# Optimization experiments

Measured on AMD Instinct MI355X. Metric: run time of the kernel, lower is better.

The kernel has to match this reference:

```python
import jax, jax.numpy as jnp
import numpy as np

NUM_HEADS = 8
OUT_FEATURES = 64
ALPHA = 0.2


def setup_inputs() -> dict:
    key = jax.random.key(0)
    k1, k2, k3, k4 = jax.random.split(key, 4)
    B, N, E, F_IN = 2, 8192, 4096, 256
    x = jax.random.normal(k1, (B, N, F_IN), dtype=jnp.float32)
    H = jax.random.uniform(k2, (N, E), dtype=jnp.float32)
    # xavier-like scaled params
    W = jax.random.normal(k3, (F_IN, OUT_FEATURES * NUM_HEADS), dtype=jnp.float32) * 0.05
    a_vertices = jax.random.normal(k4, (OUT_FEATURES, 1), dtype=jnp.float32) * 0.1
    return {"x": x, "H": H, "W": W, "a_vertices": a_vertices}


def reference(x, H, W, a_vertices):
    B, N, _ = x.shape
    # Wh: (B, N, heads, out)
    Wh = jnp.matmul(x, W).reshape(B, N, NUM_HEADS, OUT_FEATURES)
    # per-node, per-head attention logit: (B, N, heads)
    av = jax.nn.leaky_relu(jnp.einsum('bnhd,d->bnh', Wh, a_vertices[:, 0]), ALPHA)
    # edge attention: softmax over edges (torch dim=0 of (E, heads))
    ae = jax.nn.softmax(jnp.einsum('ne,bnh->beh', H, av), axis=1)  # (B, E, heads)
    # aggregate node features onto edges: (B, E, heads, out)
    m = jnp.einsum('ne,bnhd->behd', H, Wh)
    # scatter back to nodes with edge-attention weighting: (B, N, heads, out)
    out = jnp.einsum('ne,beh,behd->bnhd', H, ae, m)
    return out.reshape(B, N, NUM_HEADS * OUT_FEATURES)
```

## Files before the change

kernel.cpp:

```cpp
#include <hip/hip_runtime.h>

#define N_NODES 8192
#define N_EDGES 4096
#define F_INS   256
#define HEADS   8
#define DOUT    64
#define HDIM    512
#define CCOMB   1024
#define BATCH   2

typedef __bf16 bf16x8 __attribute__((ext_vector_type(8)));
typedef __bf16 bf16x4 __attribute__((ext_vector_type(4)));
typedef float  f32x4  __attribute__((ext_vector_type(4)));

__device__ __forceinline__ void gld_lds16(const __bf16* g, __bf16* l) {
    __builtin_amdgcn_global_load_lds(
        (const __attribute__((address_space(1))) void*)g,
        (__attribute__((address_space(3))) void*)l, 16, 0, 0);
}

__launch_bounds__(256, 4)
__global__ void convert_H_logits_kernel(const float* __restrict__ H,
                                        const float* __restrict__ av,
                                        __bf16* __restrict__ Hb,
                                        __bf16* __restrict__ HbT,
                                        float* __restrict__ plog) {
    __shared__ __align__(16) char smem[33280];
    float* lav = (float*)smem;
    __bf16 (*tile)[32][132] = (__bf16(*)[32][132])(smem + 16384);
    float* red = (float*)smem;

    int t = threadIdx.x;
    int e0 = blockIdx.x * 128;
    int n0 = blockIdx.y * 256;
    int equad = t & 31, r0 = t >> 5;
    int lane = t & 63, wv = t >> 6;

    for (int p = t; p < 4096; p += 256) {
        int n = p >> 4, q = p & 15, b = q >> 3, h = q & 7;
        lav[p] = av[(size_t)b * (N_NODES * 8) + (size_t)(n0 + n) * 8 + h];
    }

    const float* hbase = H + (size_t)n0 * N_EDGES + e0 + equad * 4;
    __bf16* hb_base = Hb + (size_t)n0 * N_EDGES + e0 + equad * 4;

    f32x4 acc[4][4] = {};

    __syncthreads();

    float4 v[4];
    for (int g = 0; g < 8; ++g) {
        int nb = g * 32;
#pragma unroll
        for (int k = 0; k < 4; ++k) {
            int n = nb + r0 + 8 * k;
            v[k] = *(const float4*)(hbase + (size_t)n * N_EDGES);
        }
        if (g > 0) {
            int pb = (g - 1) & 1, pnb = (g - 1) * 32;
#pragma unroll
            for (int s = 0; s < 2; ++s) {
                int id = s * 256 + t;
                int er = id >> 2, oct = id & 3;
                bf16x8 val;
#pragma unroll
                for (int j = 0; j < 8; ++j) val[j] = tile[pb][oct * 8 + j][er];
                *(bf16x8*)(HbT + (size_t)(e0 + er) * N_NODES + n0 + pnb + oct * 8) = val;
            }
        }
        int buf = g & 1;
#pragma unroll
        for (int k = 0; k < 4; ++k) {
            int n = nb + r0 + 8 * k;
            const f32x4* lrow = (const f32x4*)&lav[n * 16];
            float4 vv = v[k];
#pragma unroll
            for (int qq = 0; qq < 4; ++qq) {
                f32x4 l = lrow[qq];
                acc[0][qq] += l * vv.x;
                acc[1][qq] += l * vv.y;
                acc[2][qq] += l * vv.z;
                acc[3][qq] += l * vv.w;
            }
            bf16x4 hb;
            hb.x = (__bf16)vv.x; hb.y = (__bf16)vv.y;
            hb.z = (__bf16)vv.z; hb.w = (__bf16)vv.w;
            *(bf16x4*)(hb_base + (size_t)n * N_EDGES) = hb;
            *(bf16x4*)&tile[buf][r0 + 8 * k][equad * 4] = hb;
        }
        __syncthreads();
    }
    {
        int pnb = 7 * 32;
#pragma unroll
        for (int s = 0; s < 2; ++s) {
            int id = s * 256 + t;
            int er = id >> 2, oct = id & 3;
            bf16x8 val;
#pragma unroll
            for (int j = 0; j < 8; ++j) val[j] = tile[1][oct * 8 + j][er];
            *(bf16x8*)(HbT + (size_t)(e0 + er) * N_NODES + n0 + pnb + oct * 8) = val;
        }
    }

#pragma unroll
    for (int ec = 0; ec < 4; ++ec)
#pragma unroll
        for (int qq = 0; qq < 4; ++qq)
#pragma unroll
            for (int qi = 0; qi < 4; ++qi)
                acc[ec][qq][qi] += __shfl_xor(acc[ec][qq][qi], 32, 64);

    __syncthreads();
    if (lane < 32) {
#pragma unroll
        for (int qq = 0; qq < 4; ++qq)
#pragma unroll
            for (int qi = 0; qi < 4; ++qi) {
                f32x4 tmp = {acc[0][qq][qi], acc[1][qq][qi],
                             acc[2][qq][qi], acc[3][qq][qi]};
                *(f32x4*)&red[wv * 2048 + (qq * 4 + qi) * 128 + equad * 4] = tmp;
            }
    }
    __syncthreads();
#pragma unroll
    for (int s = 0; s < 8; ++s) {
        int id = s * 256 + t;
        int q = id >> 7, el = id & 127;
        float sum = red[q * 128 + el] + red[2048 + q * 128 + el] +
                    red[4096 + q * 128 + el] + red[6144 + q * 128 + el];
        plog[((size_t)blockIdx.y * 16 + q) * N_EDGES + e0 + el] = sum;
    }
}

__launch_bounds__(256)
__global__ void reduce_logits_kernel(const float* __restrict__ plog,
                                     float* __restrict__ logits) {
    int id = blockIdx.x * 256 + threadIdx.x;
    int q = id >> 12, e = id & 4095;
    float s = 0.f;
#pragma unroll
    for (int nb = 0; nb < 32; ++nb)
        s += plog[((size_t)nb * 16 + q) * N_EDGES + e];
    logits[(size_t)q * N_EDGES + e] = s;
}

__launch_bounds__(256)
__global__ void wbt_kernel(const float* __restrict__ W, __bf16* __restrict__ WbT) {
    int i = blockIdx.x * 256 + threadIdx.x;
    int c = i >> 8, f = i & 255;
    WbT[i] = (__bf16)W[(size_t)f * HDIM + c];
}

__launch_bounds__(256)
__global__ void wa_kernel(const float* __restrict__ W, const float* __restrict__ a,
                          float* __restrict__ Wa) {
    int i = blockIdx.x * 256 + threadIdx.x;
    if (i >= F_INS * HEADS) return;
    int f = i >> 3, h = i & 7;
    float s = 0.f;
#pragma unroll 8
    for (int d = 0; d < DOUT; ++d) s += W[(size_t)f * HDIM + h * DOUT + d] * a[d];
    Wa[i] = s;
}

__launch_bounds__(256)
__global__ void av_kernel(const float* __restrict__ x, const float* __restrict__ Wa,
                          float* __restrict__ av, __bf16* __restrict__ xb) {
    __shared__ float lx[32][257];
    __shared__ float lwa[F_INS * HEADS];
    int t = threadIdx.x;
    size_t row0 = (size_t)blockIdx.x * 32;
    for (int p = t; p < F_INS * HEADS; p += 256) lwa[p] = Wa[p];
#pragma unroll
    for (int p = 0; p < 32; ++p) {
        float v = x[(row0 + p) * F_INS + t];
        lx[p][t] = v;
        xb[(row0 + p) * F_INS + t] = (__bf16)v;
    }
    __syncthreads();
    int r = t >> 3, h = t & 7;
    float acc = 0.f;
#pragma unroll 8
    for (int f = 0; f < F_INS; ++f) acc += lx[r][f] * lwa[f * 8 + h];
    av[(row0 + r) * 8 + h] = acc > 0.f ? acc : 0.2f * acc;
}

__launch_bounds__(256)
__global__ void softmax_kernel(float* __restrict__ logits) {
    __shared__ float red[4];
    __shared__ float reds[4];
    int t = threadIdx.x;
    float* row = logits + (size_t)blockIdx.x * N_EDGES;
    float mx = -1e30f;
    for (int i = t; i < N_EDGES; i += 256) mx = fmaxf(mx, row[i]);
#pragma unroll
    for (int o = 32; o > 0; o >>= 1) mx = fmaxf(mx, __shfl_xor(mx, o, 64));
    if ((t & 63) == 0) red[t >> 6] = mx;
    __syncthreads();
    mx = fmaxf(fmaxf(red[0], red[1]), fmaxf(red[2], red[3]));
    float s = 0.f;
    for (int i = t; i < N_EDGES; i += 256) {
        float v = expf(row[i] - mx);
        row[i] = v;
        s += v;
    }
#pragma unroll
    for (int o = 32; o > 0; o >>= 1) s += __shfl_xor(s, o, 64);
    if ((t & 63) == 0) reds[t >> 6] = s;
    __syncthreads();
    float inv = 1.0f / (reds[0] + reds[1] + reds[2] + reds[3]);
    for (int i = t; i < N_EDGES; i += 256) row[i] *= inv;
}

template <int MODE>
__launch_bounds__(256, 4)
__global__ void gemm_bt(const __bf16* __restrict__ A, const __bf16* __restrict__ BT,
                        int lda, int ldbt, int K,
                        size_t a_bz, size_t bt_bz, size_t out_z,
                        __bf16* __restrict__ outB, int ldo,
                        float* __restrict__ outF) {
    __shared__ __bf16 AsF[8192];
    __shared__ __bf16 BsF[8192];
    int t = threadIdx.x;
    int bz = blockIdx.z;
    A  += (size_t)bz * a_bz;
    BT += (size_t)bz * bt_bz;
    if (MODE == 0) outB += (size_t)bz * out_z;
    if (MODE == 1) outF += (size_t)bz * out_z;
    size_t m0 = (size_t)blockIdx.y * 128;
    size_t n0 = (size_t)blockIdx.x * 128;

    int lane = t & 63, wv = t >> 6;
    int ln = lane & 15, lk = lane >> 4;

    const __bf16* pA[4]; const __bf16* pB[4];
    __bf16* lA[4]; __bf16* lB[4];
#pragma unroll
    for (int p = 0; p < 4; ++p) {
        int bid = wv * 4 + p;
        int mb = bid >> 1, kb = bid & 1;
        pA[p] = A + (m0 + mb * 16 + ln) * (size_t)lda + kb * 32 + lk * 8;
        pB[p] = BT + (n0 + mb * 16 + ln) * (size_t)ldbt + kb * 32 + lk * 8;
        lA[p] = &AsF[bid * 512];
        lB[p] = &BsF[bid * 512];
    }

    int wm16 = (wv & 1) * 4, wn16 = (wv >> 1) * 4;
    f32x4 acc[4][4] = {};

    for (int k0 = 0; k0 < K; k0 += 64) {
        __syncthreads();
#pragma unroll
        for (int p = 0; p < 4; ++p) gld_lds16(pA[p] + k0, lA[p]);
#pragma unroll
        for (int p = 0; p < 4; ++p) gld_lds16(pB[p] + k0, lB[p]);
        __syncthreads();
#pragma unroll
        for (int ksb = 0; ksb < 2; ++ksb) {
            bf16x8 af[4], bfr[4];
#pragma unroll
            for (int i = 0; i < 4; ++i)
                af[i] = *(const bf16x8*)&AsF[((wm16 + i) * 2 + ksb) * 512 + lane * 8];
#pragma unroll
            for (int j = 0; j < 4; ++j)
                bfr[j] = *(const bf16x8*)&BsF[((wn16 + j) * 2 + ksb) * 512 + lane * 8];
#pragma unroll
            for (int i = 0; i < 4; ++i)
#pragma unroll
                for (int j = 0; j < 4; ++j)
                    acc[i][j] = __builtin_amdgcn_mfma_f32_16x16x32_bf16(
                        af[i], bfr[j], acc[i][j], 0, 0, 0);
        }
    }

    int wm = (wv & 1) * 64, wn = (wv >> 1) * 64;
#pragma unroll
    for (int i = 0; i < 4; ++i)
#pragma unroll
        for (int j = 0; j < 4; ++j)
#pragma unroll
            for (int rg = 0; rg < 4; ++rg) {
                int gm = (int)m0 + wm + i * 16 + lk * 4 + rg;
                int gc = (int)n0 + wn + j * 16 + ln;
                float v = acc[i][j][rg];
                if (MODE == 0) {
                    outB[(size_t)gm * ldo + gc] = (__bf16)v;
                } else if (MODE == 1) {
                    outF[(size_t)gm * ldo + gc] = v;
                } else {
                    outF[(size_t)(gc >> 9) * ((size_t)N_NODES * HDIM) +
                         (size_t)gm * HDIM + (gc & 511)] = v;
                }
            }
}

template <int SWZ>
__launch_bounds__(512, 2)
__global__ void gemm256(const __bf16* __restrict__ A, const __bf16* __restrict__ BT,
                        int lda, int ldbt, int K,
                        size_t a_bz, size_t bt_bz, size_t out_z,
                        float* __restrict__ outF, int ldo) {
    __shared__ __bf16 lds[4 * 32 * 512];
    int bx, by, bz;
    if (SWZ) {
        int g = (int)blockIdx.x + 4 * ((int)blockIdx.y + 32 * (int)blockIdx.z);
        int xcd = g & 7, j = g >> 3;
        int l = (j & 3) + 4 * xcd + 32 * (j >> 2);
        bx = l & 3; by = (l >> 2) & 31; bz = l >> 7;
    } else {
        bx = blockIdx.x; by = blockIdx.y; bz = blockIdx.z;
    }
    A    += (size_t)bz * a_bz;
    BT   += (size_t)bz * bt_bz;
    outF += (size_t)bz * out_z;
    size_t m0 = (size_t)by * 256;
    size_t n0 = (size_t)bx * 256;

    int t = threadIdx.x;
    int lane = t & 63, wv = t >> 6;
    int ln = lane & 15, lk = lane >> 4;

    int fw = wv * 2;
    const __bf16* gA0 = A + (m0 + fw * 16 + ln) * (size_t)lda + lk * 8;
    const __bf16* gA1 = gA0 + 16 * (size_t)lda;
    const __bf16* gB0 = BT + (n0 + fw * 16 + ln) * (size_t)ldbt + lk * 8;
    const __bf16* gB1 = gB0 + 16 * (size_t)ldbt;

    int NT = K >> 5;

    for (int tt = 0; tt < 3; ++tt) {
        __bf16* d = &lds[tt * 16384];
        gld_lds16(gA0 + tt * 32, d + fw * 512);
        gld_lds16(gA1 + tt * 32, d + (fw + 1) * 512);
        gld_lds16(gB0 + tt * 32, d + (16 + fw) * 512);
        gld_lds16(gB1 + tt * 32, d + (16 + fw + 1) * 512);
    }
    asm volatile("s_waitcnt vmcnt(8)" ::: "memory");
    __builtin_amdgcn_s_barrier();
    __builtin_amdgcn_sched_barrier(0);

    f32x4 acc[8][4] = {};
    int wmf = (wv >> 2) * 8;
    int wnf = (wv & 3) * 4;

    auto compute = [&](int tl) {
        const __bf16* buf = &lds[(tl & 3) * 16384];
        bf16x8 af[8], bfr[4];
#pragma unroll
        for (int i = 0; i < 8; ++i)
            af[i] = *(const bf16x8*)(buf + (wmf + i) * 512 + lane * 8);
#pragma unroll
        for (int j = 0; j < 4; ++j)
            bfr[j] = *(const bf16x8*)(buf + (16 + wnf + j) * 512 + lane * 8);
        __builtin_amdgcn_s_setprio(1);
#pragma unroll
        for (int i = 0; i < 8; ++i)
#pragma unroll
            for (int j = 0; j < 4; ++j)
                acc[i][j] = __builtin_amdgcn_mfma_f32_16x16x32_bf16(
                    af[i], bfr[j], acc[i][j], 0, 0, 0);
        __builtin_amdgcn_s_setprio(0);
    };

    for (int tl = 0; tl < NT - 3; ++tl) {
        __bf16* d = &lds[((tl + 3) & 3) * 16384];
        int off = (tl + 3) * 32;
        gld_lds16(gA0 + off, d + fw * 512);
        gld_lds16(gA1 + off, d + (fw + 1) * 512);
        gld_lds16(gB0 + off, d + (16 + fw) * 512);
        gld_lds16(gB1 + off, d + (16 + fw + 1) * 512);
        compute(tl);
        asm volatile("s_waitcnt vmcnt(8)" ::: "memory");
        __builtin_amdgcn_s_barrier();
        __builtin_amdgcn_sched_barrier(0);
    }
    compute(NT - 3);
    asm volatile("s_waitcnt vmcnt(4)" ::: "memory");
    __builtin_amdgcn_s_barrier();
    __builtin_amdgcn_sched_barrier(0);
    compute(NT - 2);
    asm volatile("s_waitcnt vmcnt(0)" ::: "memory");
    __builtin_amdgcn_s_barrier();
    __builtin_amdgcn_sched_barrier(0);
    compute(NT - 1);

    int wm = (wv >> 2) * 128, wn = (wv & 3) * 64;
#pragma unroll
    for (int i = 0; i < 8; ++i)
#pragma unroll
        for (int j = 0; j < 4; ++j)
#pragma unroll
            for (int rg = 0; rg < 4; ++rg) {
                int gm = (int)m0 + wm + i * 16 + lk * 4 + rg;
                int gc = (int)n0 + wn + j * 16 + ln;
                outF[(size_t)gm * ldo + gc] = acc[i][j][rg];
            }
}

__launch_bounds__(256)
__global__ void scale1_kernel(const float* __restrict__ acc1, const float* __restrict__ ae,
                              __bf16* __restrict__ mwT) {
    int i = blockIdx.x * 256 + threadIdx.x;
    size_t base = (size_t)i * 4;
    int c = (int)(base >> 12);
    int e = (int)(base & 4095);
    const size_t slab = (size_t)CCOMB * N_EDGES / 4;
    float4 s0 = ((const float4*)acc1)[i];
    float4 s1 = ((const float4*)acc1)[i + slab];
    float4 s2 = ((const float4*)acc1)[i + 2 * slab];
    float4 s3 = ((const float4*)acc1)[i + 3 * slab];
    float4 a4 = *(const float4*)(ae + ((size_t)(c >> 6) << 12) + e);
    bf16x4 o;
    o.x = (__bf16)((s0.x + s1.x + s2.x + s3.x) * a4.x);
    o.y = (__bf16)((s0.y + s1.y + s2.y + s3.y) * a4.y);
    o.z = (__bf16)((s0.z + s1.z + s2.z + s3.z) * a4.z);
    o.w = (__bf16)((s0.w + s1.w + s2.w + s3.w) * a4.w);
    ((bf16x4*)mwT)[i] = o;
}

__launch_bounds__(256)
__global__ void reduce2_kernel(const float* __restrict__ s, float* __restrict__ out) {
    int i = blockIdx.x * 256 + threadIdx.x;
    size_t base = (size_t)i * 4;
    int m = (int)(base >> 10);
    int c = (int)(base & 1023);
    const size_t slab = (size_t)N_NODES * CCOMB / 4;
    float4 a = ((const float4*)s)[i];
    float4 b = ((const float4*)s)[i + slab];
    float4 o;
    o.x = a.x + b.x; o.y = a.y + b.y; o.z = a.z + b.z; o.w = a.w + b.w;
    *(float4*)&out[(size_t)(c >> 9) * ((size_t)N_NODES * HDIM) +
                   (size_t)m * HDIM + (c & 511)] = o;
}

extern "C" void kernel_launch(void* const* d_in, const int* in_sizes, int n_in,
                              void* d_out, int out_size, void* d_ws, size_t ws_size,
                              hipStream_t stream) {
    const float* x = (const float*)d_in[0];
    const float* H = (const float*)d_in[1];
    const float* W = (const float*)d_in[2];
    const float* a = (const float*)d_in[3];
    float* out = (float*)d_out;

    char* p = (char*)d_ws;
    __bf16* Hb   = (__bf16*)p; p += (size_t)N_NODES * N_EDGES * 2;
    __bf16* HbT  = (__bf16*)p; p += (size_t)N_EDGES * N_NODES * 2;
    __bf16* xb   = (__bf16*)p; p += (size_t)BATCH * N_NODES * F_INS * 2;
    __bf16* WbT  = (__bf16*)p; p += (size_t)HDIM * F_INS * 2;
    __bf16* WhbT = (__bf16*)p; p += (size_t)CCOMB * N_NODES * 2;
    __bf16* mwT  = (__bf16*)p; p += (size_t)CCOMB * N_EDGES * 2;
    float*  Wa   = (float*)p;  p += (size_t)F_INS * HEADS * 4;
    float*  av   = (float*)p;  p += (size_t)BATCH * N_NODES * HEADS * 4;
    float*  ae   = (float*)p;  p += (size_t)16 * N_EDGES * 4;
    float*  acc1 = (float*)p;  p += (size_t)4 * CCOMB * N_EDGES * 4;
    float*  plog = acc1;

    wbt_kernel<<<dim3(HDIM * F_INS / 256), 256, 0, stream>>>(W, WbT);
    wa_kernel<<<dim3(8), 256, 0, stream>>>(W, a, Wa);
    av_kernel<<<dim3(BATCH * N_NODES / 32), 256, 0, stream>>>(x, Wa, av, xb);
    convert_H_logits_kernel<<<dim3(N_EDGES / 128, N_NODES / 256), 256, 0, stream>>>(
        H, av, Hb, HbT, plog);
    reduce_logits_kernel<<<dim3(256), 256, 0, stream>>>(plog, ae);
    softmax_kernel<<<dim3(16), 256, 0, stream>>>(ae);

    gemm_bt<0><<<dim3(64, 4, 2), 256, 0, stream>>>(
        WbT, xb, F_INS, F_INS, F_INS,
        0, (size_t)N_NODES * F_INS, (size_t)HDIM * N_NODES,
        WhbT, N_NODES, nullptr);

    gemm256<0><<<dim3(16, 4, 4), 512, 0, stream>>>(
        WhbT, HbT, N_NODES, N_NODES, 2048,
        2048, 2048, (size_t)CCOMB * N_EDGES,
        acc1, N_EDGES);

    scale1_kernel<<<dim3(CCOMB * N_EDGES / 4 / 256), 256, 0, stream>>>(acc1, ae, mwT);

    gemm256<1><<<dim3(4, 32, 2), 512, 0, stream>>>(
        Hb, mwT, N_EDGES, N_EDGES, 2048,
        2048, 2048, (size_t)N_NODES * CCOMB,
        acc1, CCOMB);

    reduce2_kernel<<<dim3(N_NODES * CCOMB / 4 / 256), 256, 0, stream>>>(acc1, out);
}
```

Baseline: 485.3 us.

## Restructure gemm256 into 4-phase ping-pong pipeline with 64-wide K tiles

Replaces the 4-deep, 32-wide K-tile ring buffer in the 256x256 GEMM with a double buffer of 64-wide K tiles. Each K tile is split into four compute phases over quadrants of the per-wave output. Each phase issues part of the next tile's global-to-LDS loads, so loads are interleaved with MFMA work and barriers are spread more finely. The aim is to halve loop iterations and overlap memory with compute more evenly. In exchange it adds more barriers per tile and a shallower prefetch distance.

After: 476.0 us. Within noise of the previous version (-1.9%).

```diff
diff --git a/kernel.cpp b/kernel.cpp
--- a/kernel.cpp
+++ b/kernel.cpp
@@ -301,7 +301,8 @@
                         int lda, int ldbt, int K,
                         size_t a_bz, size_t bt_bz, size_t out_z,
                         float* __restrict__ outF, int ldo) {
-    __shared__ __bf16 lds[4 * 32 * 512];
+    __shared__ __bf16 lds[2 * 2 * 32 * 512];
+#define LOFF(b, op, fr) ((((b) * 2 + (op)) * 32 + (fr)) * 512)
     int bx, by, bz;
     if (SWZ) {
         int g = (int)blockIdx.x + 4 * ((int)blockIdx.y + 32 * (int)blockIdx.z);
@@ -320,70 +321,91 @@
     int t = threadIdx.x;
     int lane = t & 63, wv = t >> 6;
     int ln = lane & 15, lk = lane >> 4;
-
-    int fw = wv * 2;
-    const __bf16* gA0 = A + (m0 + fw * 16 + ln) * (size_t)lda + lk * 8;
-    const __bf16* gA1 = gA0 + 16 * (size_t)lda;
-    const __bf16* gB0 = BT + (n0 + fw * 16 + ln) * (size_t)ldbt + lk * 8;
-    const __bf16* gB1 = gB0 + 16 * (size_t)ldbt;
-
-    int NT = K >> 5;
-
-    for (int tt = 0; tt < 3; ++tt) {
-        __bf16* d = &lds[tt * 16384];
-        gld_lds16(gA0 + tt * 32, d + fw * 512);
-        gld_lds16(gA1 + tt * 32, d + (fw + 1) * 512);
-        gld_lds16(gB0 + tt * 32, d + (16 + fw) * 512);
-        gld_lds16(gB1 + tt * 32, d + (16 + fw + 1) * 512);
-    }
-    asm volatile("s_waitcnt vmcnt(8)" ::: "memory");
-    __builtin_amdgcn_s_barrier();
-    __builtin_amdgcn_sched_barrier(0);
-
-    f32x4 acc[8][4] = {};
     int wmf = (wv >> 2) * 8;
     int wnf = (wv & 3) * 4;
 
-    auto compute = [&](int tl) {
-        const __bf16* buf = &lds[(tl & 3) * 16384];
-        bf16x8 af[8], bfr[4];
-#pragma unroll
-        for (int i = 0; i < 8; ++i)
-            af[i] = *(const bf16x8*)(buf + (wmf + i) * 512 + lane * 8);
-#pragma unroll
-        for (int j = 0; j < 4; ++j)
-            bfr[j] = *(const bf16x8*)(buf + (16 + wnf + j) * 512 + lane * 8);
-        __builtin_amdgcn_s_setprio(1);
-#pragma unroll
-        for (int i = 0; i < 8; ++i)
-#pragma unroll
-            for (int j = 0; j < 4; ++j)
-                acc[i][j] = __builtin_amdgcn_mfma_f32_16x16x32_bf16(
-                    af[i], bfr[j], acc[i][j], 0, 0, 0);
-        __builtin_amdgcn_s_setprio(0);
-    };
-
-    for (int tl = 0; tl < NT - 3; ++tl) {
-        __bf16* d = &lds[((tl + 3) & 3) * 16384];
-        int off = (tl + 3) * 32;
-        gld_lds16(gA0 + off, d + fw * 512);
-        gld_lds16(gA1 + off, d + (fw + 1) * 512);
-        gld_lds16(gB0 + off, d + (16 + fw) * 512);
-        gld_lds16(gB1 + off, d + (16 + fw + 1) * 512);
-        compute(tl);
-        asm volatile("s_waitcnt vmcnt(8)" ::: "memory");
-        __builtin_amdgcn_s_barrier();
-        __builtin_amdgcn_sched_barrier(0);
-    }
-    compute(NT - 3);
+    int mbA0 = (wv < 4) ? wv : wv + 4;
+    int mbA1 = (wv < 4) ? wv + 4 : wv + 8;
+    int nbB0 = (wv >> 1) * 4 + (wv & 1);
+    int nbB1 = nbB0 + 2;
+    const __bf16* gA0 = A + (m0 + mbA0 * 16 + ln) * (size_t)lda + lk * 8;
+    const __bf16* gA1 = A + (m0 + mbA1 * 16 + ln) * (size_t)lda + lk * 8;
+    const __bf16* gB0 = BT + (n0 + nbB0 * 16 + ln) * (size_t)ldbt + lk * 8;
+    const __bf16* gB1 = BT + (n0 + nbB1 * 16 + ln) * (size_t)ldbt + lk * 8;
+
+    int NT = K >> 6;
+
+    gld_lds16(gA0, &lds[LOFF(0, 0, mbA0 * 2 + 0)]);
+    gld_lds16(gA0 + 32, &lds[LOFF(0, 0, mbA0 * 2 + 1)]);
+    gld_lds16(gB0, &lds[LOFF(0, 1, nbB0 * 2 + 0)]);
+    gld_lds16(gB0 + 32, &lds[LOFF(0, 1, nbB0 * 2 + 1)]);
+    gld_lds16(gB1, &lds[LOFF(0, 1, nbB1 * 2 + 0)]);
+    gld_lds16(gB1 + 32, &lds[LOFF(0, 1, nbB1 * 2 + 1)]);
+    gld_lds16(gA1, &lds[LOFF(0, 0, mbA1 * 2 + 0)]);
+    gld_lds16(gA1 + 32, &lds[LOFF(0, 0, mbA1 * 2 + 1)]);
     asm volatile("s_waitcnt vmcnt(4)" ::: "memory");
     __builtin_amdgcn_s_barrier();
     __builtin_amdgcn_sched_barrier(0);
-    compute(NT - 2);
-    asm volatile("s_waitcnt vmcnt(0)" ::: "memory");
-    __builtin_amdgcn_s_barrier();
-    __builtin_amdgcn_sched_barrier(0);
-    compute(NT - 1);
+
+    f32x4 acc[8][4] = {};
+
+#define PHASE(TL, P, DO_STAGE, VMN)                                            \
+    {                                                                          \
+        const int c_ = (TL) & 1;                                               \
+        bf16x8 af_[4][2], bf_[2][2];                                           \
+        _Pragma("unroll") for (int mi = 0; mi < 4; ++mi)                       \
+            _Pragma("unroll") for (int ks = 0; ks < 2; ++ks)                   \
+                af_[mi][ks] = *(const bf16x8*)&lds[                            \
+                    LOFF(c_, 0, (wmf + ((P) >> 1) * 4 + mi) * 2 + ks) + lane * 8]; \
+        _Pragma("unroll") for (int nj = 0; nj < 2; ++nj)                       \
+            _Pragma("unroll") for (int ks = 0; ks < 2; ++ks)                   \
+                bf_[nj][ks] = *(const bf16x8*)&lds[                            \
+                    LOFF(c_, 1, (wnf + ((P) & 1) * 2 + nj) * 2 + ks) + lane * 8]; \
+        if (DO_STAGE) {                                                        \
+            const int ub_ = ((TL) + 1) & 1;                                    \
+            const int ko_ = ((TL) + 1) * 64;                                   \
+            if ((P) == 0) {                                                    \
+                gld_lds16(gA0 + ko_, &lds[LOFF(ub_, 0, mbA0 * 2 + 0)]);        \
+                gld_lds16(gA0 + ko_ + 32, &lds[LOFF(ub_, 0, mbA0 * 2 + 1)]);   \
+            } else if ((P) == 1) {                                             \
+                gld_lds16(gB0 + ko_, &lds[LOFF(ub_, 1, nbB0 * 2 + 0)]);        \
+                gld_lds16(gB0 + ko_ + 32, &lds[LOFF(ub_, 1, nbB0 * 2 + 1)]);   \
+            } else if ((P) == 2) {                                             \
+                gld_lds16(gB1 + ko_, &lds[LOFF(ub_, 1, nbB1 * 2 + 0)]);        \
+                gld_lds16(gB1 + ko_ + 32, &lds[LOFF(ub_, 1, nbB1 * 2 + 1)]);   \
+            } else {                                                           \
+                gld_lds16(gA1 + ko_, &lds[LOFF(ub_, 0, mbA1 * 2 + 0)]);        \
+                gld_lds16(gA1 + ko_ + 32, &lds[LOFF(ub_, 0, mbA1 * 2 + 1)]);   \
+            }                                                                  \
+        }                                                                      \
+        if ((VMN) >= 0)                                                        \
+            asm volatile("s_waitcnt vmcnt(%0)" ::"i"(VMN) : "memory");         \
+        __builtin_amdgcn_s_barrier();                                          \
+        __builtin_amdgcn_sched_barrier(0);                                     \
+        __builtin_amdgcn_s_setprio(1);                                         \
+        _Pragma("unroll") for (int mi = 0; mi < 4; ++mi)                       \
+            _Pragma("unroll") for (int nj = 0; nj < 2; ++nj)                   \
+                _Pragma("unroll") for (int ks = 0; ks < 2; ++ks)               \
+                    acc[((P) >> 1) * 4 + mi][((P) & 1) * 2 + nj] =             \
+                        __builtin_amdgcn_mfma_f32_16x16x32_bf16(               \
+                            af_[mi][ks], bf_[nj][ks],                          \
+                            acc[((P) >> 1) * 4 + mi][((P) & 1) * 2 + nj],      \
+                            0, 0, 0);                                          \
+        __builtin_amdgcn_s_setprio(0);                                         \
+    }
+
+    for (int tl = 0; tl < NT - 1; ++tl) {
+        PHASE(tl, 0, 1, 4);
+        PHASE(tl, 1, 1, 4);
+        PHASE(tl, 2, 1, 4);
+        PHASE(tl, 3, 1, 4);
+    }
+    PHASE(NT - 1, 0, 0, 2);
+    PHASE(NT - 1, 1, 0, 0);
+    PHASE(NT - 1, 2, 0, -1);
+    PHASE(NT - 1, 3, 0, -1);
+#undef PHASE
+#undef LOFF
 
     int wm = (wv >> 2) * 128, wn = (wv & 3) * 64;
 #pragma unroll
```
